# Kernel tuning notes

Measured on AMD Instinct MI355X. Metric: run time of the kernel, lower is better.

The kernel has to match this reference:

```python
import jax, jax.numpy as jnp
import numpy as np

E, H = 512, 256  # embed_dim, hidden_dim
B, SQ, SK = 2, 512, 512


def _linear_params(k, fin, fout):
    lim = 1.0 / np.sqrt(fin)
    kw, kb = jax.random.split(k)
    W = jax.random.uniform(kw, (fin, fout), minval=-lim, maxval=lim, dtype=jnp.float32)
    b = jax.random.uniform(kb, (fout,), minval=-lim, maxval=lim, dtype=jnp.float32)
    return W, b


def setup_inputs() -> dict:
    rng = jax.random.key(0)
    ks = jax.random.split(rng, 12)
    query = jax.random.normal(ks[0], (B, SQ, E), dtype=jnp.float32)
    key = jax.random.normal(ks[1], (B, SK, E), dtype=jnp.float32)
    Wqe, bqe = _linear_params(ks[2], E, H)
    Wke, bke = _linear_params(ks[3], E, H)
    W1, b1 = _linear_params(ks[4], 2 * H, H)  # importance_predictor layer 0
    W2, b2 = _linear_params(ks[5], H, H)      # layer 1
    W3, b3 = _linear_params(ks[6], H, H)      # layer 2
    Wf, bf = _linear_params(ks[7], H, 1)      # final importance logit
    Wv1, bv1 = _linear_params(ks[8], 2 * H, H)  # variance_estimator layer 0
    Wv2, bv2 = _linear_params(ks[9], H, 1)      # variance_estimator final
    return {"query": query, "key": key,
            "Wqe": Wqe, "bqe": bqe, "Wke": Wke, "bke": bke,
            "W1": W1, "b1": b1, "W2": W2, "b2": b2, "W3": W3, "b3": b3,
            "Wf": Wf, "bf": bf, "Wv1": Wv1, "bv1": bv1, "Wv2": Wv2, "bv2": bv2}


def reference(query, key, Wqe, bqe, Wke, bke, W1, b1, W2, b2, W3, b3, Wf, bf, Wv1, bv1, Wv2, bv2):
    # Encoders (dropout is identity at eval)
    qf = jax.nn.relu(jnp.einsum('bqe,eh->bqh', query, Wqe) + bqe)  # [B,Sq,H]
    kf = jax.nn.relu(jnp.einsum('bke,eh->bkh', key, Wke) + bke)    # [B,Sk,H]

    # First Linear(2H,H) on cat([q,k]) == q@W1[:H] + k@W1[H:]; broadcast over pairs
    qp = jnp.einsum('bqh,hd->bqd', qf, W1[:H])
    kp = jnp.einsum('bkh,hd->bkd', kf, W1[H:])
    h = jax.nn.relu(qp[:, :, None, :] + kp[:, None, :, :] + b1)  # [B,Sq,Sk,H]
    h = jax.nn.relu(jnp.einsum('bqkh,hd->bqkd', h, W2) + b2)
    h = jax.nn.relu(jnp.einsum('bqkh,hd->bqkd', h, W3) + b3)
    importance_logits = (jnp.einsum('bqkh,ho->bqko', h, Wf) + bf)[..., 0]  # [B,Sq,Sk]

    # Variance head: Linear(2H,H) split the same way, ReLU, Linear, Softplus
    vq = jnp.einsum('bqh,hd->bqd', qf, Wv1[:H])
    vk = jnp.einsum('bkh,hd->bkd', kf, Wv1[H:])
    v = jax.nn.relu(vq[:, :, None, :] + vk[:, None, :, :] + bv1)  # [B,Sq,Sk,H]
    estimated_variance = jax.nn.softplus((jnp.einsum('bqkh,ho->bqko', v, Wv2) + bv2)[..., 0])
    return importance_logits, estimated_variance
```

## Files before the change

kernel.cpp:

```cpp
#include <hip/hip_runtime.h>
#include <cstdint>
#include <cstddef>

#define HDIM 256
#define EDIM 512
#define NB   2
#define NSQ  512
#define NSK  512

typedef __bf16 bf16x8 __attribute__((ext_vector_type(8)));
typedef float  f32x4  __attribute__((ext_vector_type(4)));
typedef unsigned short u16x8 __attribute__((ext_vector_type(8)));

#define OFF_W2F  0u
#define OFF_W3F  65536u
#define OFF_WQEF 131072u
#define OFF_WKEF 262144u
#define OFF_WCQ  393216u
#define OFF_WCK  524288u
#define BF16_WS_END_BYTES 1310720u

__device__ __forceinline__ unsigned short f2bf(float f) {
  unsigned u = __float_as_uint(f);
  u += 0x7fffu + ((u >> 16) & 1u);
  return (unsigned short)(u >> 16);
}
__device__ __forceinline__ float relu_(float x) { return x > 0.f ? x : 0.f; }
__device__ __forceinline__ float softplus_(float x) {
  return fmaxf(x, 0.f) + log1pf(expf(-fabsf(x)));
}

__global__ __launch_bounds__(64) void shuffle_weights(
    const float* __restrict__ Wqe, const float* __restrict__ Wke,
    const float* __restrict__ W1,  const float* __restrict__ Wv1,
    const float* __restrict__ W2,  const float* __restrict__ W3,
    unsigned short* __restrict__ wsb)
{
  const int bx = blockIdx.x;
  const int lane = threadIdx.x;
  const float* src; unsigned short* dst; int S; int idx;
  if      (bx <  128) { src = W2;          dst = wsb + OFF_W2F;           S = 8;  idx = bx;        }
  else if (bx <  256) { src = W3;          dst = wsb + OFF_W3F;           S = 8;  idx = bx - 128;  }
  else if (bx <  512) { src = Wqe;         dst = wsb + OFF_WQEF;          S = 16; idx = bx - 256;  }
  else if (bx <  768) { src = Wke;         dst = wsb + OFF_WKEF;          S = 16; idx = bx - 512;  }
  else if (bx <  896) { src = W1;          dst = wsb + OFF_WCQ;           S = 8;  idx = bx - 768;  }
  else if (bx < 1024) { src = Wv1;         dst = wsb + OFF_WCQ + 65536u;  S = 8;  idx = bx - 896;  }
  else if (bx < 1152) { src = W1 + 65536;  dst = wsb + OFF_WCK;           S = 8;  idx = bx - 1024; }
  else                { src = Wv1 + 65536; dst = wsb + OFF_WCK + 65536u;  S = 8;  idx = bx - 1152; }
  const int t = idx / S, s = idx % S;
  const int n  = t * 16 + (lane & 15);
  const int k0 = s * 32 + ((lane >> 4) << 3);
  unsigned short* o = dst + ((size_t)(t * S + s) * 64 + lane) * 8;
  #pragma unroll
  for (int j = 0; j < 8; ++j)
    o[j] = f2bf(src[(size_t)(k0 + j) * 256 + n]);
}

__global__ __launch_bounds__(256) void encoder_kernel(
    const float* __restrict__ query, const float* __restrict__ key,
    const float* __restrict__ bqe,   const float* __restrict__ bke,
    const float* __restrict__ b1,    const float* __restrict__ bv1,
    const unsigned short* __restrict__ WqeF, const unsigned short* __restrict__ WkeF,
    const unsigned short* __restrict__ WcqF, const unsigned short* __restrict__ WckF,
    float* __restrict__ Pq, float* __restrict__ Pk)
{
  __shared__ unsigned short sX[32 * 520];
  __shared__ unsigned short sF[32 * 264];
  __shared__ float sBe[256];
  __shared__ float sBc[512];

  const int bx   = blockIdx.x;
  const int side = bx >> 5;
  const int rt   = bx & 31;
  const int t    = threadIdx.x;

  const float* Xsrc = side ? key : query;
  const unsigned short* WeF = side ? WkeF : WqeF;
  const unsigned short* WcF = side ? WckF : WcqF;
  float* P = side ? Pk : Pq;

  {
    const int m = t >> 3, ch = t & 7;
    const int c0 = ch * 64;
    const float* xr = Xsrc + (size_t)(rt * 32 + m) * EDIM;
    #pragma unroll
    for (int cc = 0; cc < 64; cc += 4) {
      const int c = c0 + cc;
      float4 xv = *(const float4*)(xr + c);
      ushort4 xb;
      xb.x = f2bf(xv.x); xb.y = f2bf(xv.y); xb.z = f2bf(xv.z); xb.w = f2bf(xv.w);
      *(ushort4*)&sX[m * 520 + c] = xb;
    }
    sBe[t]       = side ? bke[t] : bqe[t];
    sBc[t]       = side ? 0.f : b1[t];
    sBc[256 + t] = side ? 0.f : bv1[t];
  }
  __syncthreads();

  const int wave = t >> 6, lane = t & 63;
  const int l15 = lane & 15, q4 = lane >> 4;

  f32x4 acc1[4][2];
  #pragma unroll
  for (int ft = 0; ft < 4; ++ft)
    #pragma unroll
    for (int pt = 0; pt < 2; ++pt)
      acc1[ft][pt] = (f32x4){0.f, 0.f, 0.f, 0.f};

  for (int s = 0; s < 16; ++s) {
    bf16x8 af[4], bfr[2];
    #pragma unroll
    for (int ft = 0; ft < 4; ++ft) {
      const int tg = wave * 4 + ft;
      af[ft] = *(const bf16x8*)(WeF + ((size_t)(tg * 16 + s) * 64 + lane) * 8);
    }
    #pragma unroll
    for (int pt = 0; pt < 2; ++pt)
      bfr[pt] = *(const bf16x8*)&sX[(pt * 16 + l15) * 520 + s * 32 + q4 * 8];
    #pragma unroll
    for (int ft = 0; ft < 4; ++ft)
      #pragma unroll
      for (int pt = 0; pt < 2; ++pt)
        acc1[ft][pt] = __builtin_amdgcn_mfma_f32_16x16x32_bf16(af[ft], bfr[pt], acc1[ft][pt], 0, 0, 0);
  }

  #pragma unroll
  for (int ft = 0; ft < 4; ++ft) {
    const int tg = wave * 4 + ft;
    const int n0 = tg * 16 + q4 * 4;
    float4 b4 = *(const float4*)&sBe[n0];
    #pragma unroll
    for (int pt = 0; pt < 2; ++pt) {
      const int mr = pt * 16 + l15;
      f32x4 a = acc1[ft][pt];
      ushort4 h;
      h.x = f2bf(relu_(a[0] + b4.x));
      h.y = f2bf(relu_(a[1] + b4.y));
      h.z = f2bf(relu_(a[2] + b4.z));
      h.w = f2bf(relu_(a[3] + b4.w));
      *(ushort4*)&sF[mr * 264 + n0] = h;
    }
  }
  __syncthreads();

  f32x4 acc2[8][2];
  #pragma unroll
  for (int ft = 0; ft < 8; ++ft)
    #pragma unroll
    for (int pt = 0; pt < 2; ++pt)
      acc2[ft][pt] = (f32x4){0.f, 0.f, 0.f, 0.f};

  for (int s = 0; s < 8; ++s) {
    bf16x8 af[8], bfr[2];
    #pragma unroll
    for (int ft = 0; ft < 8; ++ft) {
      const int tg = wave * 8 + ft;
      af[ft] = *(const bf16x8*)(WcF + ((size_t)(tg * 8 + s) * 64 + lane) * 8);
    }
    #pragma unroll
    for (int pt = 0; pt < 2; ++pt)
      bfr[pt] = *(const bf16x8*)&sF[(pt * 16 + l15) * 264 + s * 32 + q4 * 8];
    #pragma unroll
    for (int ft = 0; ft < 8; ++ft)
      #pragma unroll
      for (int pt = 0; pt < 2; ++pt)
        acc2[ft][pt] = __builtin_amdgcn_mfma_f32_16x16x32_bf16(af[ft], bfr[pt], acc2[ft][pt], 0, 0, 0);
  }

  #pragma unroll
  for (int ft = 0; ft < 8; ++ft) {
    const int tg = wave * 8 + ft;
    const int n0 = tg * 16 + q4 * 4;
    float4 bc = *(const float4*)&sBc[n0];
    #pragma unroll
    for (int pt = 0; pt < 2; ++pt) {
      const int mr = pt * 16 + l15;
      const int row = rt * 32 + mr;
      f32x4 a = acc2[ft][pt];
      float4 o;
      o.x = a[0] + bc.x; o.y = a[1] + bc.y; o.z = a[2] + bc.z; o.w = a[3] + bc.w;
      *(float4*)&P[(size_t)row * 512 + n0] = o;
    }
  }
}

__global__ __launch_bounds__(512, 6) void pair_kernel(
    const float* __restrict__ Pq, const float* __restrict__ Pk,
    const unsigned short* __restrict__ W2F, const unsigned short* __restrict__ W3F,
    const float* __restrict__ b2, const float* __restrict__ b3,
    const float* __restrict__ Wf, const float* __restrict__ bfp,
    const float* __restrict__ Wv2, const float* __restrict__ bv2p,
    float* __restrict__ out)
{
  __shared__ __align__(16) unsigned char smem[37888];
  unsigned short* sXH = (unsigned short*)smem;
  float* sB2   = (float*)(smem + 32768);
  float* sB3   = (float*)(smem + 33792);
  float* sWf   = (float*)(smem + 34816);
  float* sVred = (float*)(smem + 35840);
  float* sRed  = (float*)(smem + 32768);

  const int kt = blockIdx.x, qy = blockIdx.y, bz = blockIdx.z;
  const int t = threadIdx.x;
  const float* qpRow = Pq + (size_t)(bz * NSQ + qy) * 512;

  {
    const int m   = t >> 3;
    const int sub = t & 7;
    const float* kpRow = Pk + (size_t)(bz * NSK + kt * 64 + m) * 512;
    const int msw = (m & 7);
    float vpart = 0.f;
    #pragma unroll
    for (int it = 0; it < 4; ++it) {
      const int c = it * 64 + sub * 8;
      float4 q0 = *(const float4*)(qpRow + c);
      float4 q1 = *(const float4*)(qpRow + c + 4);
      float4 k0 = *(const float4*)(kpRow + c);
      float4 k1 = *(const float4*)(kpRow + c + 4);
      u16x8 hb;
      hb[0] = f2bf(relu_(q0.x + k0.x));
      hb[1] = f2bf(relu_(q0.y + k0.y));
      hb[2] = f2bf(relu_(q0.z + k0.z));
      hb[3] = f2bf(relu_(q0.w + k0.w));
      hb[4] = f2bf(relu_(q1.x + k1.x));
      hb[5] = f2bf(relu_(q1.y + k1.y));
      hb[6] = f2bf(relu_(q1.z + k1.z));
      hb[7] = f2bf(relu_(q1.w + k1.w));
      const int chunk = (c >> 3) ^ msw;
      *(u16x8*)&sXH[m * 256 + chunk * 8] = hb;
      float4 a0 = *(const float4*)(qpRow + 256 + c);
      float4 a1 = *(const float4*)(qpRow + 256 + c + 4);
      float4 v0 = *(const float4*)(kpRow + 256 + c);
      float4 v1 = *(const float4*)(kpRow + 256 + c + 4);
      float4 w0 = *(const float4*)(Wv2 + c);
      float4 w1 = *(const float4*)(Wv2 + c + 4);
      vpart += relu_(a0.x + v0.x) * w0.x + relu_(a0.y + v0.y) * w0.y
             + relu_(a0.z + v0.z) * w0.z + relu_(a0.w + v0.w) * w0.w
             + relu_(a1.x + v1.x) * w1.x + relu_(a1.y + v1.y) * w1.y
             + relu_(a1.z + v1.z) * w1.z + relu_(a1.w + v1.w) * w1.w;
    }
    sVred[m * 8 + sub] = vpart;
    if (t < 256) { sB2[t] = b2[t]; sB3[t] = b3[t]; sWf[t] = Wf[t]; }
  }
  __syncthreads();

  const int wave = t >> 6, lane = t & 63;
  const int l15 = lane & 15, q4 = lane >> 4;
  const int lsw = l15 & 7;

  f32x4 acc[2][4];
  #pragma unroll
  for (int ft = 0; ft < 2; ++ft)
    #pragma unroll
    for (int pt = 0; pt < 4; ++pt)
      acc[ft][pt] = (f32x4){0.f, 0.f, 0.f, 0.f};

  #pragma unroll
  for (int s = 0; s < 8; ++s) {
    bf16x8 af[2], bfr[4];
    #pragma unroll
    for (int ft = 0; ft < 2; ++ft) {
      const int tg = wave * 2 + ft;
      af[ft] = *(const bf16x8*)(W2F + ((size_t)(tg * 8 + s) * 64 + lane) * 8);
    }
    #pragma unroll
    for (int pt = 0; pt < 4; ++pt) {
      const int chunk = ((s << 2) + q4) ^ lsw;
      bfr[pt] = *(const bf16x8*)&sXH[(pt * 16 + l15) * 256 + chunk * 8];
    }
    #pragma unroll
    for (int ft = 0; ft < 2; ++ft)
      #pragma unroll
      for (int pt = 0; pt < 4; ++pt)
        acc[ft][pt] = __builtin_amdgcn_mfma_f32_16x16x32_bf16(af[ft], bfr[pt], acc[ft][pt], 0, 0, 0);
  }
  __syncthreads();

  #pragma unroll
  for (int ft = 0; ft < 2; ++ft) {
    const int tg = wave * 2 + ft;
    const int n0 = tg * 16 + q4 * 4;
    float4 b4 = *(const float4*)&sB2[n0];
    const int chunkS = ((n0 >> 3) ^ lsw);
    #pragma unroll
    for (int pt = 0; pt < 4; ++pt) {
      const int mr = pt * 16 + l15;
      f32x4 a = acc[ft][pt];
      ushort4 h;
      h.x = f2bf(relu_(a[0] + b4.x));
      h.y = f2bf(relu_(a[1] + b4.y));
      h.z = f2bf(relu_(a[2] + b4.z));
      h.w = f2bf(relu_(a[3] + b4.w));
      *(ushort4*)&sXH[mr * 256 + chunkS * 8 + (n0 & 7)] = h;
    }
  }
  __syncthreads();

  f32x4 acc2[2][4];
  #pragma unroll
  for (int ft = 0; ft < 2; ++ft)
    #pragma unroll
    for (int pt = 0; pt < 4; ++pt)
      acc2[ft][pt] = (f32x4){0.f, 0.f, 0.f, 0.f};

  #pragma unroll
  for (int s = 0; s < 8; ++s) {
    bf16x8 af[2], bfr[4];
    #pragma unroll
    for (int ft = 0; ft < 2; ++ft) {
      const int tg = wave * 2 + ft;
      af[ft] = *(const bf16x8*)(W3F + ((size_t)(tg * 8 + s) * 64 + lane) * 8);
    }
    #pragma unroll
    for (int pt = 0; pt < 4; ++pt) {
      const int chunk = ((s << 2) + q4) ^ lsw;
      bfr[pt] = *(const bf16x8*)&sXH[(pt * 16 + l15) * 256 + chunk * 8];
    }
    #pragma unroll
    for (int ft = 0; ft < 2; ++ft)
      #pragma unroll
      for (int pt = 0; pt < 4; ++pt)
        acc2[ft][pt] = __builtin_amdgcn_mfma_f32_16x16x32_bf16(af[ft], bfr[pt], acc2[ft][pt], 0, 0, 0);
  }

  float p[4] = {0.f, 0.f, 0.f, 0.f};
  #pragma unroll
  for (int ft = 0; ft < 2; ++ft) {
    const int tg = wave * 2 + ft;
    const int n0 = tg * 16 + q4 * 4;
    float4 b4 = *(const float4*)&sB3[n0];
    float4 w4 = *(const float4*)&sWf[n0];
    #pragma unroll
    for (int pt = 0; pt < 4; ++pt) {
      f32x4 a = acc2[ft][pt];
      p[pt] += relu_(a[0] + b4.x) * w4.x + relu_(a[1] + b4.y) * w4.y
             + relu_(a[2] + b4.z) * w4.z + relu_(a[3] + b4.w) * w4.w;
    }
  }
  __syncthreads();
  #pragma unroll
  for (int pt = 0; pt < 4; ++pt) {
    float v = p[pt];
    v += __shfl_xor(v, 16, 64);
    v += __shfl_xor(v, 32, 64);
    if (lane < 16) sRed[wave * 64 + pt * 16 + lane] = v;
  }
  __syncthreads();

  if (t < 64) {
    const size_t o = (size_t)(bz * NSQ + qy) * NSK + kt * 64 + t;
    float lg = bfp[0];
    #pragma unroll
    for (int w = 0; w < 8; ++w) lg += sRed[w * 64 + t];
    out[o] = lg;
    float vs = bv2p[0];
    #pragma unroll
    for (int j = 0; j < 8; ++j) vs += sVred[t * 8 + j];
    out[(size_t)NB * NSQ * NSK + o] = softplus_(vs);
  }
}

extern "C" void kernel_launch(void* const* d_in, const int* in_sizes, int n_in,
                              void* d_out, int out_size, void* d_ws, size_t ws_size,
                              hipStream_t stream)
{
  (void)in_sizes; (void)n_in; (void)out_size; (void)ws_size;
  const float* query = (const float*)d_in[0];
  const float* key   = (const float*)d_in[1];
  const float* Wqe   = (const float*)d_in[2];
  const float* bqe   = (const float*)d_in[3];
  const float* Wke   = (const float*)d_in[4];
  const float* bke   = (const float*)d_in[5];
  const float* W1    = (const float*)d_in[6];
  const float* b1    = (const float*)d_in[7];
  const float* W2    = (const float*)d_in[8];
  const float* b2    = (const float*)d_in[9];
  const float* W3    = (const float*)d_in[10];
  const float* b3    = (const float*)d_in[11];
  const float* Wf    = (const float*)d_in[12];
  const float* bf    = (const float*)d_in[13];
  const float* Wv1   = (const float*)d_in[14];
  const float* bv1   = (const float*)d_in[15];
  const float* Wv2   = (const float*)d_in[16];
  const float* bv2   = (const float*)d_in[17];

  unsigned short* wsb = (unsigned short*)d_ws;
  float* Pq = (float*)((char*)d_ws + BF16_WS_END_BYTES);
  float* Pk = Pq + (size_t)1024 * 512;
  float* out = (float*)d_out;

  shuffle_weights<<<1280, 64, 0, stream>>>(Wqe, Wke, W1, Wv1, W2, W3, wsb);
  encoder_kernel<<<64, 256, 0, stream>>>(query, key, bqe, bke, b1, bv1,
      wsb + OFF_WQEF, wsb + OFF_WKEF, wsb + OFF_WCQ, wsb + OFF_WCK, Pq, Pk);
  pair_kernel<<<dim3(NSK / 64, NSQ, NB), 512, 0, stream>>>(Pq, Pk,
      wsb + OFF_W2F, wsb + OFF_W3F, b2, b3, Wf, bf, Wv2, bv2, out);
}
```

Baseline: 285.9 us.

## Halve pair-kernel block size, give each wave more MFMA tiles, use packed bf16 conversion

The pair kernel moves from 512 to 256 threads per block. Each wave now computes 4 output-feature tiles instead of 2, so every B-fragment read from LDS feeds more MFMAs. The variance reduction now uses lane shuffles and writes the output directly instead of going through shared memory, which removes one buffer and one barrier. Float-to-bf16 conversion now uses the packed two-element intrinsic throughout. The trade-offs are more accumulator registers per thread and fewer waves per block to hide latency.

```diff
diff --git a/kernel.cpp b/kernel.cpp
--- a/kernel.cpp
+++ b/kernel.cpp
@@ -1,4 +1,5 @@
 #include <hip/hip_runtime.h>
+#include <hip/hip_bf16.h>
 #include <cstdint>
 #include <cstddef>
 
@@ -24,6 +25,10 @@
   unsigned u = __float_as_uint(f);
   u += 0x7fffu + ((u >> 16) & 1u);
   return (unsigned short)(u >> 16);
+}
+__device__ __forceinline__ ushort2 f2bf2(float x, float y) {
+  __hip_bfloat162 h = __float22bfloat162_rn(float2{x, y});
+  return *(ushort2*)&h;
 }
 __device__ __forceinline__ float relu_(float x) { return x > 0.f ? x : 0.f; }
 __device__ __forceinline__ float softplus_(float x) {
@@ -52,8 +57,10 @@
   const int k0 = s * 32 + ((lane >> 4) << 3);
   unsigned short* o = dst + ((size_t)(t * S + s) * 64 + lane) * 8;
   #pragma unroll
-  for (int j = 0; j < 8; ++j)
-    o[j] = f2bf(src[(size_t)(k0 + j) * 256 + n]);
+  for (int j = 0; j < 8; j += 2) {
+    ushort2 pp = f2bf2(src[(size_t)(k0 + j) * 256 + n], src[(size_t)(k0 + j + 1) * 256 + n]);
+    *(ushort2*)&o[j] = pp;
+  }
 }
 
 __global__ __launch_bounds__(256) void encoder_kernel(
@@ -87,8 +94,9 @@
     for (int cc = 0; cc < 64; cc += 4) {
       const int c = c0 + cc;
       float4 xv = *(const float4*)(xr + c);
-      ushort4 xb;
-      xb.x = f2bf(xv.x); xb.y = f2bf(xv.y); xb.z = f2bf(xv.z); xb.w = f2bf(xv.w);
+      ushort2 lo = f2bf2(xv.x, xv.y);
+      ushort2 hi = f2bf2(xv.z, xv.w);
+      ushort4 xb; xb.x = lo.x; xb.y = lo.y; xb.z = hi.x; xb.w = hi.y;
       *(ushort4*)&sX[m * 520 + c] = xb;
     }
     sBe[t]       = side ? bke[t] : bqe[t];
@@ -133,11 +141,9 @@
     for (int pt = 0; pt < 2; ++pt) {
       const int mr = pt * 16 + l15;
       f32x4 a = acc1[ft][pt];
-      ushort4 h;
-      h.x = f2bf(relu_(a[0] + b4.x));
-      h.y = f2bf(relu_(a[1] + b4.y));
-      h.z = f2bf(relu_(a[2] + b4.z));
-      h.w = f2bf(relu_(a[3] + b4.w));
+      ushort2 lo = f2bf2(relu_(a[0] + b4.x), relu_(a[1] + b4.y));
+      ushort2 hi = f2bf2(relu_(a[2] + b4.z), relu_(a[3] + b4.w));
+      ushort4 h; h.x = lo.x; h.y = lo.y; h.z = hi.x; h.w = hi.y;
       *(ushort4*)&sF[mr * 264 + n0] = h;
     }
   }
@@ -184,7 +190,7 @@
   }
 }
 
-__global__ __launch_bounds__(512, 6) void pair_kernel(
+__global__ __launch_bounds__(256, 4) void pair_kernel(
     const float* __restrict__ Pq, const float* __restrict__ Pk,
     const unsigned short* __restrict__ W2F, const unsigned short* __restrict__ W3F,
     const float* __restrict__ b2, const float* __restrict__ b3,
@@ -192,12 +198,11 @@
     const float* __restrict__ Wv2, const float* __restrict__ bv2p,
     float* __restrict__ out)
 {
-  __shared__ __align__(16) unsigned char smem[37888];
+  __shared__ __align__(16) unsigned char smem[35840];
   unsigned short* sXH = (unsigned short*)smem;
   float* sB2   = (float*)(smem + 32768);
   float* sB3   = (float*)(smem + 33792);
   float* sWf   = (float*)(smem + 34816);
-  float* sVred = (float*)(smem + 35840);
   float* sRed  = (float*)(smem + 32768);
 
   const int kt = blockIdx.x, qy = blockIdx.y, bz = blockIdx.z;
@@ -205,28 +210,26 @@
   const float* qpRow = Pq + (size_t)(bz * NSQ + qy) * 512;
 
   {
-    const int m   = t >> 3;
-    const int sub = t & 7;
+    const int m   = t >> 2;
+    const int sub = t & 3;
     const float* kpRow = Pk + (size_t)(bz * NSK + kt * 64 + m) * 512;
     const int msw = (m & 7);
     float vpart = 0.f;
     #pragma unroll
-    for (int it = 0; it < 4; ++it) {
-      const int c = it * 64 + sub * 8;
+    for (int it = 0; it < 8; ++it) {
+      const int c = sub * 64 + it * 8;
       float4 q0 = *(const float4*)(qpRow + c);
       float4 q1 = *(const float4*)(qpRow + c + 4);
       float4 k0 = *(const float4*)(kpRow + c);
       float4 k1 = *(const float4*)(kpRow + c + 4);
+      ushort2 p0 = f2bf2(relu_(q0.x + k0.x), relu_(q0.y + k0.y));
+      ushort2 p1 = f2bf2(relu_(q0.z + k0.z), relu_(q0.w + k0.w));
+      ushort2 p2 = f2bf2(relu_(q1.x + k1.x), relu_(q1.y + k1.y));
+      ushort2 p3 = f2bf2(relu_(q1.z + k1.z), relu_(q1.w + k1.w));
       u16x8 hb;
-      hb[0] = f2bf(relu_(q0.x + k0.x));
-      hb[1] = f2bf(relu_(q0.y + k0.y));
-      hb[2] = f2bf(relu_(q0.z + k0.z));
-      hb[3] = f2bf(relu_(q0.w + k0.w));
-      hb[4] = f2bf(relu_(q1.x + k1.x));
-      hb[5] = f2bf(relu_(q1.y + k1.y));
-      hb[6] = f2bf(relu_(q1.z + k1.z));
-      hb[7] = f2bf(relu_(q1.w + k1.w));
-      const int chunk = (c >> 3) ^ msw;
+      hb[0] = p0.x; hb[1] = p0.y; hb[2] = p1.x; hb[3] = p1.y;
+      hb[4] = p2.x; hb[5] = p2.y; hb[6] = p3.x; hb[7] = p3.y;
+      const int chunk = (sub * 8 + it) ^ msw;
       *(u16x8*)&sXH[m * 256 + chunk * 8] = hb;
       float4 a0 = *(const float4*)(qpRow + 256 + c);
       float4 a1 = *(const float4*)(qpRow + 256 + c + 4);
@@ -239,8 +242,13 @@
              + relu_(a1.x + v1.x) * w1.x + relu_(a1.y + v1.y) * w1.y
              + relu_(a1.z + v1.z) * w1.z + relu_(a1.w + v1.w) * w1.w;
     }
-    sVred[m * 8 + sub] = vpart;
-    if (t < 256) { sB2[t] = b2[t]; sB3[t] = b3[t]; sWf[t] = Wf[t]; }
+    vpart += __shfl_xor(vpart, 1, 64);
+    vpart += __shfl_xor(vpart, 2, 64);
+    if (sub == 0) {
+      const size_t o = (size_t)(bz * NSQ + qy) * NSK + kt * 64 + m;
+      out[(size_t)NB * NSQ * NSK + o] = softplus_(vpart + bv2p[0]);
+    }
+    sB2[t] = b2[t]; sB3[t] = b3[t]; sWf[t] = Wf[t];
   }
   __syncthreads();
 
@@ -248,19 +256,19 @@
   const int l15 = lane & 15, q4 = lane >> 4;
   const int lsw = l15 & 7;
 
-  f32x4 acc[2][4];
-  #pragma unroll
-  for (int ft = 0; ft < 2; ++ft)
+  f32x4 acc[4][4];
+  #pragma unroll
+  for (int ft = 0; ft < 4; ++ft)
     #pragma unroll
     for (int pt = 0; pt < 4; ++pt)
       acc[ft][pt] = (f32x4){0.f, 0.f, 0.f, 0.f};
 
   #pragma unroll
   for (int s = 0; s < 8; ++s) {
-    bf16x8 af[2], bfr[4];
-    #pragma unroll
-    for (int ft = 0; ft < 2; ++ft) {
-      const int tg = wave * 2 + ft;
+    bf16x8 af[4], bfr[4];
+    #pragma unroll
+    for (int ft = 0; ft < 4; ++ft) {
+      const int tg = wave * 4 + ft;
       af[ft] = *(const bf16x8*)(W2F + ((size_t)(tg * 8 + s) * 64 + lane) * 8);
     }
     #pragma unroll
@@ -269,7 +277,7 @@
       bfr[pt] = *(const bf16x8*)&sXH[(pt * 16 + l15) * 256 + chunk * 8];
     }
     #pragma unroll
-    for (int ft = 0; ft < 2; ++ft)
+    for (int ft = 0; ft < 4; ++ft)
       #pragma unroll
       for (int pt = 0; pt < 4; ++pt)
         acc[ft][pt] = __builtin_amdgcn_mfma_f32_16x16x32_bf16(af[ft], bfr[pt], acc[ft][pt], 0, 0, 0);
@@ -277,8 +285,8 @@
   __syncthreads();
 
   #pragma unroll
-  for (int ft = 0; ft < 2; ++ft) {
-    const int tg = wave * 2 + ft;
+  for (int ft = 0; ft < 4; ++ft) {
+    const int tg = wave * 4 + ft;
     const int n0 = tg * 16 + q4 * 4;
     float4 b4 = *(const float4*)&sB2[n0];
     const int chunkS = ((n0 >> 3) ^ lsw);
@@ -286,29 +294,27 @@
     for (int pt = 0; pt < 4; ++pt) {
       const int mr = pt * 16 + l15;
       f32x4 a = acc[ft][pt];
-      ushort4 h;
-      h.x = f2bf(relu_(a[0] + b4.x));
-      h.y = f2bf(relu_(a[1] + b4.y));
-      h.z = f2bf(relu_(a[2] + b4.z));
-      h.w = f2bf(relu_(a[3] + b4.w));
+      ushort2 lo = f2bf2(relu_(a[0] + b4.x), relu_(a[1] + b4.y));
+      ushort2 hi = f2bf2(relu_(a[2] + b4.z), relu_(a[3] + b4.w));
+      ushort4 h; h.x = lo.x; h.y = lo.y; h.z = hi.x; h.w = hi.y;
       *(ushort4*)&sXH[mr * 256 + chunkS * 8 + (n0 & 7)] = h;
     }
   }
   __syncthreads();
 
-  f32x4 acc2[2][4];
-  #pragma unroll
-  for (int ft = 0; ft < 2; ++ft)
+  f32x4 acc2[4][4];
+  #pragma unroll
+  for (int ft = 0; ft < 4; ++ft)
     #pragma unroll
     for (int pt = 0; pt < 4; ++pt)
       acc2[ft][pt] = (f32x4){0.f, 0.f, 0.f, 0.f};
 
   #pragma unroll
   for (int s = 0; s < 8; ++s) {
-    bf16x8 af[2], bfr[4];
-    #pragma unroll
-    for (int ft = 0; ft < 2; ++ft) {
-      const int tg = wave * 2 + ft;
+    bf16x8 af[4], bfr[4];
+    #pragma unroll
+    for (int ft = 0; ft < 4; ++ft) {
+      const int tg = wave * 4 + ft;
       af[ft] = *(const bf16x8*)(W3F + ((size_t)(tg * 8 + s) * 64 + lane) * 8);
     }
     #pragma unroll
@@ -317,7 +323,7 @@
       bfr[pt] = *(const bf16x8*)&sXH[(pt * 16 + l15) * 256 + chunk * 8];
     }
     #pragma unroll
-    for (int ft = 0; ft < 2; ++ft)
+    for (int ft = 0; ft < 4; ++ft)
       #pragma unroll
       for (int pt = 0; pt < 4; ++pt)
         acc2[ft][pt] = __builtin_amdgcn_mfma_f32_16x16x32_bf16(af[ft], bfr[pt], acc2[ft][pt], 0, 0, 0);
@@ -325,8 +331,8 @@
 
   float p[4] = {0.f, 0.f, 0.f, 0.f};
   #pragma unroll
-  for (int ft = 0; ft < 2; ++ft) {
-    const int tg = wave * 2 + ft;
+  for (int ft = 0; ft < 4; ++ft) {
+    const int tg = wave * 4 + ft;
     const int n0 = tg * 16 + q4 * 4;
     float4 b4 = *(const float4*)&sB3[n0];
     float4 w4 = *(const float4*)&sWf[n0];
@@ -337,7 +343,6 @@
              + relu_(a[2] + b4.z) * w4.z + relu_(a[3] + b4.w) * w4.w;
     }
   }
-  __syncthreads();
   #pragma unroll
   for (int pt = 0; pt < 4; ++pt) {
     float v = p[pt];
@@ -349,14 +354,8 @@
 
   if (t < 64) {
     const size_t o = (size_t)(bz * NSQ + qy) * NSK + kt * 64 + t;
-    float lg = bfp[0];
-    #pragma unroll
-    for (int w = 0; w < 8; ++w) lg += sRed[w * 64 + t];
+    float lg = bfp[0] + sRed[t] + sRed[64 + t] + sRed[128 + t] + sRed[192 + t];
     out[o] = lg;
-    float vs = bv2p[0];
-    #pragma unroll
-    for (int j = 0; j < 8; ++j) vs += sVred[t * 8 + j];
-    out[(size_t)NB * NSQ * NSK + o] = softplus_(vs);
   }
 }
 
@@ -392,6 +391,6 @@
   shuffle_weights<<<1280, 64, 0, stream>>>(Wqe, Wke, W1, Wv1, W2, W3, wsb);
   encoder_kernel<<<64, 256, 0, stream>>>(query, key, bqe, bke, b1, bv1,
       wsb + OFF_WQEF, wsb + OFF_WKEF, wsb + OFF_WCQ, wsb + OFF_WCK, Pq, Pk);
-  pair_kernel<<<dim3(NSK / 64, NSQ, NB), 512, 0, stream>>>(Pq, Pk,
+  pair_kernel<<<dim3(NSK / 64, NSQ, NB), 256, 0, stream>>>(Pq, Pk,
       wsb + OFF_W2F, wsb + OFF_W3F, b2, b3, Wf, bf, Wv2, bv2, out);
 }
```

Measured after the change: 470.5 us. 64.6% more time.
